# Kernel optimization log

Measured on AMD Instinct MI355X. Metric: run time of the kernel, lower is better.

## Reference

```python
import jax, jax.numpy as jnp
import numpy as np

N_NODES = 1_000_000
D_IN = 128
GRAPH_STATE_DIM = 128  # node_hidden_sizes[-1] before doubling
N_GRAPHS = 4096


def setup_inputs() -> dict:
    key = jax.random.key(0)
    ks = jax.random.split(key, 10)
    s = lambda fan_in: 1.0 / np.sqrt(fan_in)
    return {
        "node_states": jax.random.normal(ks[0], (N_NODES, D_IN), dtype=jnp.float32),
        "graph_idx": jax.random.randint(ks[1], (N_NODES,), 0, N_GRAPHS),
        # MLP1: D_IN -> 64 -> 2*GRAPH_STATE_DIM
        "W1": jax.random.uniform(ks[2], (D_IN, 64), jnp.float32, -s(D_IN), s(D_IN)),
        "b1": jnp.zeros((64,), jnp.float32),
        "W2": jax.random.uniform(ks[3], (64, 2 * GRAPH_STATE_DIM), jnp.float32, -s(64), s(64)),
        "b2": jnp.zeros((2 * GRAPH_STATE_DIM,), jnp.float32),
        # MLP2: GRAPH_STATE_DIM -> 32 -> 16
        "W3": jax.random.uniform(ks[4], (GRAPH_STATE_DIM, 32), jnp.float32, -s(GRAPH_STATE_DIM), s(GRAPH_STATE_DIM)),
        "b3": jnp.zeros((32,), jnp.float32),
        "W4": jax.random.uniform(ks[5], (32, 16), jnp.float32, -s(32), s(32)),
        "b4": jnp.zeros((16,), jnp.float32),
    }


def reference(node_states, graph_idx, W1, b1, W2, b2, W3, b3, W4, b4):
    # MLP1: [N, D_IN] -> [N, 2*GRAPH_STATE_DIM]
    h = jax.nn.relu(node_states @ W1 + b1) @ W2 + b2
    gates = jax.nn.sigmoid(h[:, :GRAPH_STATE_DIM])
    gated = h[:, GRAPH_STATE_DIM:] * gates  # [N, GRAPH_STATE_DIM]
    # unsorted segment sum over graphs (n_graphs = max(graph_idx)+1 = N_GRAPHS)
    graph_states = jax.ops.segment_sum(gated, graph_idx, num_segments=N_GRAPHS)
    # MLP2: [G, GRAPH_STATE_DIM] -> [G, 16]
    out = jax.nn.relu(graph_states @ W3 + b3) @ W4 + b4
    return out
```

## Files before the change

### kernel.cpp

```cpp
#include <hip/hip_runtime.h>
#include <hip/hip_bf16.h>

#define N_NODES 1000000
#define D_IN 128
#define NG 4096
#define GSD 128
#define NPAD_MAX (N_NODES + NG * 31)
#define NGROUP_MAX 35232
#define K5_BLOCKS 8808

typedef __attribute__((ext_vector_type(4))) float f32x4;
typedef __attribute__((ext_vector_type(8))) short bf16x8;
typedef __attribute__((ext_vector_type(4))) int i32x4;

__device__ __forceinline__ short f2bs(float f) {
    unsigned u = __float_as_uint(f);
    u += 0x7FFF + ((u >> 16) & 1);
    return (short)(u >> 16);
}

__device__ __forceinline__ float sigmoid_fast(float x) {
    float e = __builtin_amdgcn_exp2f(-1.44269504089f * x);
    return __builtin_amdgcn_rcpf(1.0f + e);
}

__global__ void wconv_kernel(const float* __restrict__ W1, const float* __restrict__ W2,
                             short* __restrict__ w1t, short* __restrict__ w2t) {
    int idx = blockIdx.x * 256 + threadIdx.x;
    if (idx < 8192) {
        int n = idx >> 7, k = idx & 127;
        w1t[idx] = f2bs(W1[k * 64 + n]);
    } else {
        int j = idx - 8192;
        int n = j >> 6, k = j & 63;
        w2t[j] = f2bs(W2[k * 256 + n]);
    }
}

__global__ void hist_kernel(const int* __restrict__ gidx, int* __restrict__ cnt) {
    __shared__ int h[NG];
    int t = threadIdx.x;
    for (int i = t; i < NG; i += 256) h[i] = 0;
    __syncthreads();
    for (int i = blockIdx.x * 256 + t; i < N_NODES; i += gridDim.x * 256)
        atomicAdd(&h[gidx[i]], 1);
    __syncthreads();
    for (int i = t; i < NG; i += 256) {
        int v = h[i];
        if (v) atomicAdd(&cnt[i], v);
    }
}

__global__ __launch_bounds__(1024) void scan_kernel(const int* __restrict__ cnt,
                                                    int* __restrict__ poff,
                                                    int* __restrict__ ggid) {
    __shared__ int sc[1024];
    int t = threadIdx.x;
    int c[4];
    int s = 0;
#pragma unroll
    for (int i = 0; i < 4; ++i) {
        int cc = cnt[t * 4 + i];
        c[i] = (cc + 31) & ~31;
        s += c[i];
    }
    sc[t] = s;
    __syncthreads();
    for (int off = 1; off < 1024; off <<= 1) {
        int v = (t >= off) ? sc[t - off] : 0;
        __syncthreads();
        sc[t] += v;
        __syncthreads();
    }
    int base = sc[t] - s;
#pragma unroll
    for (int i = 0; i < 4; ++i) {
        int g = t * 4 + i;
        poff[g] = base;
        int ngp = c[i] >> 5;
        int gb = base >> 5;
        for (int k = 0; k < ngp; ++k) ggid[gb + k] = g;
        base += c[i];
    }
}

__global__ void scatter_kernel(const int* __restrict__ gidx, const int* __restrict__ poff,
                               int* __restrict__ cur, int* __restrict__ order) {
    int i = blockIdx.x * 256 + threadIdx.x;
    if (i >= N_NODES) return;
    int g = gidx[i];
    int p = atomicAdd(&cur[g], 1);
    order[poff[g] + p] = i;
}

__global__ __launch_bounds__(256, 2) void main_kernel(
        const float* __restrict__ X, const short* __restrict__ w1t,
        const short* __restrict__ w2t, const float* __restrict__ b1,
        const float* __restrict__ b2, const int* __restrict__ order,
        const int* __restrict__ ggid, float* __restrict__ gs) {
    __shared__ __align__(16) short lds[36352];
    const int tid = threadIdx.x;

    for (int ci = tid; ci < 1024; ci += 256) {
        int n = ci >> 4, cp = ci & 15;
        *(i32x4*)&lds[n * 136 + cp * 8] = *(const i32x4*)&w1t[n * 128 + cp * 8];
    }
    for (int ci = tid; ci < 2048; ci += 256) {
        int n = ci >> 3, cp = ci & 7;
        *(i32x4*)&lds[8704 + n * 72 + cp * 8] = *(const i32x4*)&w2t[n * 64 + cp * 8];
    }
    __syncthreads();

    const int w = (blockIdx.x << 2) + (tid >> 6);
    const int lane = tid & 63;
    const int l15 = lane & 15;
    const int q = lane >> 4;
    const int h1base = 27136 + (tid >> 6) * 2304;
    const int g = ggid[w];
    const bool active = (g >= 0);
    unsigned rowmask = 0;

    if (active) {
        int nd0 = order[w * 32 + l15];
        int nd1 = order[w * 32 + 16 + l15];
        unsigned long long m0 = __ballot(nd0 >= 0);
        unsigned long long m1 = __ballot(nd1 >= 0);
        rowmask = ((unsigned)(m1 & 0xFFFFULL) << 16) | (unsigned)(m0 & 0xFFFFULL);
        bool v0 = nd0 >= 0, v1 = nd1 >= 0;
        const float* xp0 = X + (long long)(v0 ? nd0 : 0) * D_IN;
        const float* xp1 = X + (long long)(v1 ? nd1 : 0) * D_IN;

        f32x4 acc1[2][4];
#pragma unroll
        for (int mt = 0; mt < 2; ++mt)
#pragma unroll
            for (int nt = 0; nt < 4; ++nt) acc1[mt][nt] = (f32x4){0.f, 0.f, 0.f, 0.f};

        const f32x4 z = {0.f, 0.f, 0.f, 0.f};
#pragma unroll
        for (int kk = 0; kk < 4; ++kk) {
            int koff = kk * 32 + q * 8;
            f32x4 x00 = v0 ? *(const f32x4*)(xp0 + koff) : z;
            f32x4 x01 = v0 ? *(const f32x4*)(xp0 + koff + 4) : z;
            f32x4 x10 = v1 ? *(const f32x4*)(xp1 + koff) : z;
            f32x4 x11 = v1 ? *(const f32x4*)(xp1 + koff + 4) : z;
            bf16x8 a0, a1;
#pragma unroll
            for (int j = 0; j < 4; ++j) {
                a0[j] = f2bs(x00[j]); a0[4 + j] = f2bs(x01[j]);
                a1[j] = f2bs(x10[j]); a1[4 + j] = f2bs(x11[j]);
            }
#pragma unroll
            for (int nt = 0; nt < 4; ++nt) {
                bf16x8 b = *(const bf16x8*)&lds[(nt * 16 + l15) * 136 + koff];
                acc1[0][nt] = __builtin_amdgcn_mfma_f32_16x16x32_bf16(a0, b, acc1[0][nt], 0, 0, 0);
                acc1[1][nt] = __builtin_amdgcn_mfma_f32_16x16x32_bf16(a1, b, acc1[1][nt], 0, 0, 0);
            }
        }
#pragma unroll
        for (int nt = 0; nt < 4; ++nt) {
            float bb = b1[nt * 16 + l15];
#pragma unroll
            for (int mt = 0; mt < 2; ++mt)
#pragma unroll
                for (int r = 0; r < 4; ++r) {
                    float h = fmaxf(acc1[mt][nt][r] + bb, 0.f);
                    lds[h1base + (mt * 16 + q * 4 + r) * 72 + nt * 16 + l15] = f2bs(h);
                }
        }
    }
    __syncthreads();
    if (active) {
        f32x4 acc2[2][16];
#pragma unroll
        for (int mt = 0; mt < 2; ++mt)
#pragma unroll
            for (int nt = 0; nt < 16; ++nt) acc2[mt][nt] = (f32x4){0.f, 0.f, 0.f, 0.f};

#pragma unroll
        for (int ks = 0; ks < 2; ++ks) {
            int koff = ks * 32 + q * 8;
            bf16x8 a0 = *(const bf16x8*)&lds[h1base + l15 * 72 + koff];
            bf16x8 a1 = *(const bf16x8*)&lds[h1base + (16 + l15) * 72 + koff];
#pragma unroll
            for (int nt = 0; nt < 16; ++nt) {
                bf16x8 b = *(const bf16x8*)&lds[8704 + (nt * 16 + l15) * 72 + koff];
                acc2[0][nt] = __builtin_amdgcn_mfma_f32_16x16x32_bf16(a0, b, acc2[0][nt], 0, 0, 0);
                acc2[1][nt] = __builtin_amdgcn_mfma_f32_16x16x32_bf16(a1, b, acc2[1][nt], 0, 0, 0);
            }
        }
#pragma unroll
        for (int nt = 0; nt < 8; ++nt) {
            float bg = b2[nt * 16 + l15];
            float bv = b2[128 + nt * 16 + l15];
            float s = 0.f;
#pragma unroll
            for (int mt = 0; mt < 2; ++mt)
#pragma unroll
                for (int r = 0; r < 4; ++r) {
                    int row = mt * 16 + q * 4 + r;
                    float gate = sigmoid_fast(acc2[mt][nt][r] + bg);
                    float val = acc2[mt][nt + 8][r] + bv;
                    float gv = gate * val;
                    s += ((rowmask >> row) & 1u) ? gv : 0.f;
                }
            s += __shfl_xor(s, 16);
            s += __shfl_xor(s, 32);
            if (lane < 16) unsafeAtomicAdd(&gs[(long long)g * GSD + nt * 16 + l15], s);
        }
    }
}

__global__ void mlp2_kernel(const float* __restrict__ gs, const float* __restrict__ W3,
                            const float* __restrict__ b3, const float* __restrict__ W4,
                            const float* __restrict__ b4, float* __restrict__ out) {
    __shared__ __align__(16) float sgs[8 * 128];
    __shared__ float sh3[8 * 32];
    int t = threadIdx.x;
    int g0 = blockIdx.x * 8;
    *(f32x4*)&sgs[t * 4] = *(const f32x4*)(gs + (long long)g0 * 128 + t * 4);
    __syncthreads();
    {
        int li = t >> 5, j = t & 31;
        float acc = b3[j];
#pragma unroll 8
        for (int k = 0; k < 128; ++k) acc += sgs[li * 128 + k] * W3[k * 32 + j];
        sh3[li * 32 + j] = fmaxf(acc, 0.f);
    }
    __syncthreads();
    if (t < 128) {
        int li = t >> 4, o = t & 15;
        float acc = b4[o];
#pragma unroll
        for (int j = 0; j < 32; ++j) acc += sh3[li * 32 + j] * W4[j * 16 + o];
        out[(g0 + li) * 16 + o] = acc;
    }
}

extern "C" void kernel_launch(void* const* d_in, const int* in_sizes, int n_in,
                              void* d_out, int out_size, void* d_ws, size_t ws_size,
                              hipStream_t stream) {
    (void)in_sizes; (void)n_in; (void)out_size; (void)ws_size;
    const float* X  = (const float*)d_in[0];
    const int* gidx = (const int*)d_in[1];
    const float* W1 = (const float*)d_in[2];
    const float* b1 = (const float*)d_in[3];
    const float* W2 = (const float*)d_in[4];
    const float* b2 = (const float*)d_in[5];
    const float* W3 = (const float*)d_in[6];
    const float* b3 = (const float*)d_in[7];
    const float* W4 = (const float*)d_in[8];
    const float* b4 = (const float*)d_in[9];
    float* out = (float*)d_out;

    char* ws   = (char*)d_ws;
    float* gs  = (float*)(ws + 0);
    int* cnt   = (int*)(ws + 2097152);
    int* cur   = (int*)(ws + 2113536);
    int* poff  = (int*)(ws + 2129920);
    int* ggid  = (int*)(ws + 2146304);
    short* w1t = (short*)(ws + 2287232);
    short* w2t = (short*)(ws + 2303616);
    int* order = (int*)(ws + 2336384);

    hipMemsetAsync(ws, 0, 2146304, stream);
    hipMemsetAsync(ws + 2146304, 0xFF, 140928, stream);
    hipMemsetAsync(ws + 2336384, 0xFF, 4507904, stream);

    wconv_kernel<<<96, 256, 0, stream>>>(W1, W2, w1t, w2t);
    hist_kernel<<<512, 256, 0, stream>>>(gidx, cnt);
    scan_kernel<<<1, 1024, 0, stream>>>(cnt, poff, ggid);
    scatter_kernel<<<(N_NODES + 255) / 256, 256, 0, stream>>>(gidx, poff, cur, order);
    main_kernel<<<K5_BLOCKS, 256, 0, stream>>>(X, w1t, w2t, b1, b2, order, ggid, gs);
    mlp2_kernel<<<512, 256, 0, stream>>>(gs, W3, b3, W4, b4, out);
}
```

Baseline: 901.7 us.

## Swizzle LDS layouts, encode row counts in group ids, drop padding memsets

Replaces padded LDS strides with XOR-swizzled layouts for W1, W2 and the hidden tile, and reuses the W1 region for hidden activations. That cuts LDS per block so occupancy can rise to 3 blocks per CU. The second GEMM now computes gate and value tiles per output chunk instead of holding all 32 accumulators, which lowers register pressure. Valid row counts are packed into ggid and the group count is stored in meta, so the large 0xFF memsets of order and ggid are removed. The trade-off is an extra __syncthreads and more complex index math.

```diff
diff --git a/kernel.cpp b/kernel.cpp
--- a/kernel.cpp
+++ b/kernel.cpp
@@ -5,7 +5,6 @@
 #define D_IN 128
 #define NG 4096
 #define GSD 128
-#define NPAD_MAX (N_NODES + NG * 31)
 #define NGROUP_MAX 35232
 #define K5_BLOCKS 8808
 
@@ -28,12 +27,14 @@
                              short* __restrict__ w1t, short* __restrict__ w2t) {
     int idx = blockIdx.x * 256 + threadIdx.x;
     if (idx < 8192) {
-        int n = idx >> 7, k = idx & 127;
+        int n = idx >> 7, rem = idx & 127, c = rem >> 3, j = rem & 7;
+        int k = ((c ^ (n & 15)) << 3) | j;
         w1t[idx] = f2bs(W1[k * 64 + n]);
     } else {
-        int j = idx - 8192;
-        int n = j >> 6, k = j & 63;
-        w2t[j] = f2bs(W2[k * 256 + n]);
+        int s = idx - 8192;
+        int n = s >> 6, rem = s & 63, c = rem >> 3, j = rem & 7;
+        int k = ((c ^ (n & 7)) << 3) | j;
+        w2t[s] = f2bs(W2[k * 256 + n]);
     }
 }
 
@@ -53,15 +54,16 @@
 
 __global__ __launch_bounds__(1024) void scan_kernel(const int* __restrict__ cnt,
                                                     int* __restrict__ poff,
-                                                    int* __restrict__ ggid) {
+                                                    int* __restrict__ ggid,
+                                                    int* __restrict__ meta) {
     __shared__ int sc[1024];
     int t = threadIdx.x;
-    int c[4];
+    int cc[4], c[4];
     int s = 0;
 #pragma unroll
     for (int i = 0; i < 4; ++i) {
-        int cc = cnt[t * 4 + i];
-        c[i] = (cc + 31) & ~31;
+        cc[i] = cnt[t * 4 + i];
+        c[i] = (cc[i] + 31) & ~31;
         s += c[i];
     }
     sc[t] = s;
@@ -72,6 +74,7 @@
         sc[t] += v;
         __syncthreads();
     }
+    if (t == 1023) meta[0] = sc[1023] >> 5;
     int base = sc[t] - s;
 #pragma unroll
     for (int i = 0; i < 4; ++i) {
@@ -79,7 +82,11 @@
         poff[g] = base;
         int ngp = c[i] >> 5;
         int gb = base >> 5;
-        for (int k = 0; k < ngp; ++k) ggid[gb + k] = g;
+        for (int k = 0; k < ngp; ++k) {
+            int rem = cc[i] - k * 32;
+            int rows = rem > 32 ? 32 : rem;
+            ggid[gb + k] = (g << 6) | (rows - 1);
+        }
         base += c[i];
     }
 }
@@ -93,44 +100,46 @@
     order[poff[g] + p] = i;
 }
 
-__global__ __launch_bounds__(256, 2) void main_kernel(
+__global__ __launch_bounds__(256, 3) void main_kernel(
         const float* __restrict__ X, const short* __restrict__ w1t,
         const short* __restrict__ w2t, const float* __restrict__ b1,
         const float* __restrict__ b2, const int* __restrict__ order,
-        const int* __restrict__ ggid, float* __restrict__ gs) {
-    __shared__ __align__(16) short lds[36352];
+        const int* __restrict__ ggid, const int* __restrict__ meta,
+        float* __restrict__ gs) {
+    __shared__ __align__(16) short lds[24576];
     const int tid = threadIdx.x;
 
-    for (int ci = tid; ci < 1024; ci += 256) {
-        int n = ci >> 4, cp = ci & 15;
-        *(i32x4*)&lds[n * 136 + cp * 8] = *(const i32x4*)&w1t[n * 128 + cp * 8];
-    }
-    for (int ci = tid; ci < 2048; ci += 256) {
-        int n = ci >> 3, cp = ci & 7;
-        *(i32x4*)&lds[8704 + n * 72 + cp * 8] = *(const i32x4*)&w2t[n * 64 + cp * 8];
-    }
-    __syncthreads();
-
-    const int w = (blockIdx.x << 2) + (tid >> 6);
+    for (int ci = tid; ci < 2048; ci += 256)
+        *(i32x4*)&lds[ci * 8] = *(const i32x4*)&w2t[ci * 8];
+    for (int ci = tid; ci < 1024; ci += 256)
+        *(i32x4*)&lds[16384 + ci * 8] = *(const i32x4*)&w1t[ci * 8];
+
+    const int wid = tid >> 6;
+    const int w = (blockIdx.x << 2) + wid;
     const int lane = tid & 63;
     const int l15 = lane & 15;
     const int q = lane >> 4;
-    const int h1base = 27136 + (tid >> 6) * 2304;
-    const int g = ggid[w];
-    const bool active = (g >= 0);
+    const int ngroups = meta[0];
+    const bool active = (w < ngroups);
+
+    int g = 0, rows = 0;
     unsigned rowmask = 0;
+    f32x4 acc1[2][4];
+
+    __syncthreads();
 
     if (active) {
-        int nd0 = order[w * 32 + l15];
-        int nd1 = order[w * 32 + 16 + l15];
-        unsigned long long m0 = __ballot(nd0 >= 0);
-        unsigned long long m1 = __ballot(nd1 >= 0);
-        rowmask = ((unsigned)(m1 & 0xFFFFULL) << 16) | (unsigned)(m0 & 0xFFFFULL);
-        bool v0 = nd0 >= 0, v1 = nd1 >= 0;
-        const float* xp0 = X + (long long)(v0 ? nd0 : 0) * D_IN;
-        const float* xp1 = X + (long long)(v1 ? nd1 : 0) * D_IN;
-
-        f32x4 acc1[2][4];
+        int enc = ggid[w];
+        g = enc >> 6;
+        rows = (enc & 63) + 1;
+        rowmask = (rows >= 32) ? 0xFFFFFFFFu : ((1u << rows) - 1u);
+        bool v0 = l15 < rows;
+        bool v1 = (16 + l15) < rows;
+        int nd0r = order[w * 32 + l15];
+        int nd1r = order[w * 32 + 16 + l15];
+        const float* xp0 = X + (long long)(v0 ? nd0r : 0) * D_IN;
+        const float* xp1 = X + (long long)(v1 ? nd1r : 0) * D_IN;
+
 #pragma unroll
         for (int mt = 0; mt < 2; ++mt)
 #pragma unroll
@@ -150,60 +159,74 @@
                 a0[j] = f2bs(x00[j]); a0[4 + j] = f2bs(x01[j]);
                 a1[j] = f2bs(x10[j]); a1[4 + j] = f2bs(x11[j]);
             }
+            int ch = (kk * 4 + q);
 #pragma unroll
             for (int nt = 0; nt < 4; ++nt) {
-                bf16x8 b = *(const bf16x8*)&lds[(nt * 16 + l15) * 136 + koff];
+                bf16x8 b = *(const bf16x8*)&lds[16384 + (nt * 16 + l15) * 128 + ((ch ^ l15) << 3)];
                 acc1[0][nt] = __builtin_amdgcn_mfma_f32_16x16x32_bf16(a0, b, acc1[0][nt], 0, 0, 0);
                 acc1[1][nt] = __builtin_amdgcn_mfma_f32_16x16x32_bf16(a1, b, acc1[1][nt], 0, 0, 0);
             }
         }
+    }
+
+    __syncthreads();
+
+    const int h1b = 16384 + wid * 2048;
+    if (active) {
 #pragma unroll
         for (int nt = 0; nt < 4; ++nt) {
             float bb = b1[nt * 16 + l15];
+            int c = nt * 2 + (l15 >> 3);
+            int j7 = l15 & 7;
 #pragma unroll
             for (int mt = 0; mt < 2; ++mt)
 #pragma unroll
                 for (int r = 0; r < 4; ++r) {
+                    int m = mt * 16 + q * 4 + r;
                     float h = fmaxf(acc1[mt][nt][r] + bb, 0.f);
-                    lds[h1base + (mt * 16 + q * 4 + r) * 72 + nt * 16 + l15] = f2bs(h);
+                    lds[h1b + m * 64 + ((c ^ (m & 7)) << 3) + j7] = f2bs(h);
                 }
         }
     }
-    __syncthreads();
+
+    __syncthreads();
+
     if (active) {
-        f32x4 acc2[2][16];
-#pragma unroll
-        for (int mt = 0; mt < 2; ++mt)
-#pragma unroll
-            for (int nt = 0; nt < 16; ++nt) acc2[mt][nt] = (f32x4){0.f, 0.f, 0.f, 0.f};
-
+        bf16x8 A0[2], A1[2];
 #pragma unroll
         for (int ks = 0; ks < 2; ++ks) {
-            int koff = ks * 32 + q * 8;
-            bf16x8 a0 = *(const bf16x8*)&lds[h1base + l15 * 72 + koff];
-            bf16x8 a1 = *(const bf16x8*)&lds[h1base + (16 + l15) * 72 + koff];
-#pragma unroll
-            for (int nt = 0; nt < 16; ++nt) {
-                bf16x8 b = *(const bf16x8*)&lds[8704 + (nt * 16 + l15) * 72 + koff];
-                acc2[0][nt] = __builtin_amdgcn_mfma_f32_16x16x32_bf16(a0, b, acc2[0][nt], 0, 0, 0);
-                acc2[1][nt] = __builtin_amdgcn_mfma_f32_16x16x32_bf16(a1, b, acc2[1][nt], 0, 0, 0);
-            }
+            int ch = ((ks * 4 + q) ^ (l15 & 7)) << 3;
+            A0[ks] = *(const bf16x8*)&lds[h1b + l15 * 64 + ch];
+            A1[ks] = *(const bf16x8*)&lds[h1b + (16 + l15) * 64 + ch];
         }
 #pragma unroll
         for (int nt = 0; nt < 8; ++nt) {
+            f32x4 aG0 = (f32x4){0.f, 0.f, 0.f, 0.f}, aG1 = aG0, aV0 = aG0, aV1 = aG0;
+#pragma unroll
+            for (int ks = 0; ks < 2; ++ks) {
+                int ch = ((ks * 4 + q) ^ (l15 & 7)) << 3;
+                bf16x8 bG = *(const bf16x8*)&lds[(nt * 16 + l15) * 64 + ch];
+                bf16x8 bV = *(const bf16x8*)&lds[((nt + 8) * 16 + l15) * 64 + ch];
+                aG0 = __builtin_amdgcn_mfma_f32_16x16x32_bf16(A0[ks], bG, aG0, 0, 0, 0);
+                aG1 = __builtin_amdgcn_mfma_f32_16x16x32_bf16(A1[ks], bG, aG1, 0, 0, 0);
+                aV0 = __builtin_amdgcn_mfma_f32_16x16x32_bf16(A0[ks], bV, aV0, 0, 0, 0);
+                aV1 = __builtin_amdgcn_mfma_f32_16x16x32_bf16(A1[ks], bV, aV1, 0, 0, 0);
+            }
             float bg = b2[nt * 16 + l15];
             float bv = b2[128 + nt * 16 + l15];
             float s = 0.f;
 #pragma unroll
-            for (int mt = 0; mt < 2; ++mt)
+            for (int mt = 0; mt < 2; ++mt) {
+                f32x4 aG = mt ? aG1 : aG0;
+                f32x4 aV = mt ? aV1 : aV0;
 #pragma unroll
                 for (int r = 0; r < 4; ++r) {
                     int row = mt * 16 + q * 4 + r;
-                    float gate = sigmoid_fast(acc2[mt][nt][r] + bg);
-                    float val = acc2[mt][nt + 8][r] + bv;
-                    float gv = gate * val;
+                    float gate = sigmoid_fast(aG[r] + bg);
+                    float gv = gate * (aV[r] + bv);
                     s += ((rowmask >> row) & 1u) ? gv : 0.f;
                 }
+            }
             s += __shfl_xor(s, 16);
             s += __shfl_xor(s, 32);
             if (lane < 16) unsafeAtomicAdd(&gs[(long long)g * GSD + nt * 16 + l15], s);
@@ -258,19 +281,18 @@
     int* cnt   = (int*)(ws + 2097152);
     int* cur   = (int*)(ws + 2113536);
     int* poff  = (int*)(ws + 2129920);
-    int* ggid  = (int*)(ws + 2146304);
-    short* w1t = (short*)(ws + 2287232);
-    short* w2t = (short*)(ws + 2303616);
-    int* order = (int*)(ws + 2336384);
-
-    hipMemsetAsync(ws, 0, 2146304, stream);
-    hipMemsetAsync(ws + 2146304, 0xFF, 140928, stream);
-    hipMemsetAsync(ws + 2336384, 0xFF, 4507904, stream);
+    int* meta  = (int*)(ws + 2146304);
+    short* w1t = (short*)(ws + 2146368);
+    short* w2t = (short*)(ws + 2162752);
+    int* ggid  = (int*)(ws + 2195520);
+    int* order = (int*)(ws + 2336448);
+
+    hipMemsetAsync(ws, 0, 2129920, stream);
 
     wconv_kernel<<<96, 256, 0, stream>>>(W1, W2, w1t, w2t);
     hist_kernel<<<512, 256, 0, stream>>>(gidx, cnt);
-    scan_kernel<<<1, 1024, 0, stream>>>(cnt, poff, ggid);
+    scan_kernel<<<1, 1024, 0, stream>>>(cnt, poff, ggid, meta);
     scatter_kernel<<<(N_NODES + 255) / 256, 256, 0, stream>>>(gidx, poff, cur, order);
-    main_kernel<<<K5_BLOCKS, 256, 0, stream>>>(X, w1t, w2t, b1, b2, order, ggid, gs);
+    main_kernel<<<K5_BLOCKS, 256, 0, stream>>>(X, w1t, w2t, b1, b2, order, ggid, meta, gs);
     mlp2_kernel<<<512, 256, 0, stream>>>(gs, W3, b3, W4, b4, out);
 }
```

New measurement: 860.6 us. 1.05x faster.
